# Optimization experiments

Hardware: AMD Instinct MI355X
Metric: run time of the kernel (lower is better)

## Reference

```python
import jax, jax.numpy as jnp
import numpy as np

N_ITERS = 30  # sinkhorn iterations, matching torch default


def sinkhorn(log_alpha, n_iters=N_ITERS):
    # log_alpha: (B, N, K) -> approximately doubly-stochastic (B, N, K)
    x = log_alpha - jnp.max(log_alpha, axis=(-2, -1), keepdims=True)
    x = jnp.exp(x)
    for _ in range(n_iters):
        x = x / (jnp.sum(x, axis=-1, keepdims=True) + 1e-8)  # row normalize
        x = x / (jnp.sum(x, axis=-2, keepdims=True) + 1e-8)  # col normalize
    return x


def greedy_unique_argmax(scores):
    # scores: (B, N, K) with N == K. Returns hard permutation matrix (B, N, K).
    B, N, K = scores.shape

    def one(s):  # s: (N, K)
        order = jnp.argsort(-s.reshape(-1))  # flat indices, descending score

        def body(carry, idx):
            used_r, used_c, assign = carry
            r = idx // K
            c = idx % K
            take = jnp.logical_not(used_r[r] | used_c[c])
            used_r = used_r.at[r].set(used_r[r] | take)
            used_c = used_c.at[c].set(used_c[c] | take)
            assign = assign.at[r].set(jnp.where(take, c, assign[r]))
            return (used_r, used_c, assign), None

        init = (jnp.zeros((N,), jnp.bool_),
                jnp.zeros((K,), jnp.bool_),
                jnp.full((N,), 0, jnp.int32))
        (_, _, assign), _ = jax.lax.scan(body, init, order)
        return jax.nn.one_hot(assign, K, dtype=s.dtype)

    return jax.vmap(one)(scores)


def setup_inputs() -> dict:
    key = jax.random.key(0)
    B, N, K = 4096, 64, 64
    cell_logits = jax.random.normal(key, (B, N, K), dtype=jnp.float32)
    pos_temp = jnp.asarray(1.1, dtype=jnp.float32)  # softplus(pos_temp_raw)+1e-6 at init
    return {"cell_logits": cell_logits, "pos_temp": pos_temp}


def reference(cell_logits, pos_temp):
    logits = cell_logits / (pos_temp + 1e-6)
    w_soft = sinkhorn(logits, N_ITERS)
    w_hard = greedy_unique_argmax(jax.lax.stop_gradient(w_soft))
    # straight-through: forward = hard permutation, backward = soft sinkhorn grads
    w = w_hard + (w_soft - jax.lax.stop_gradient(w_soft))
    return w
```

## Files before the change

kernel.cpp:

```cpp
#include <hip/hip_runtime.h>
#include <cstdint>
#include <cstddef>


typedef float f2 __attribute__((ext_vector_type(2)));

__device__ __forceinline__ f2 fma2(f2 a, f2 b, f2 c) {
#if defined(__has_builtin) && __has_builtin(__builtin_elementwise_fma)
    return __builtin_elementwise_fma(a, b, c);
#else
    f2 r; r.x = __builtin_fmaf(a.x, b.x, c.x); r.y = __builtin_fmaf(a.y, b.y, c.y);
    return r;
#endif
}

__global__ void __launch_bounds__(64)
__attribute__((amdgpu_waves_per_eu(1)))
sinkhorn_perm_kernel(const float* __restrict__ logits,
                     const float* __restrict__ ptemp,
                     float* __restrict__ out)
{
    __shared__ __attribute__((aligned(16))) float bufU[64];
    __shared__ __attribute__((aligned(16))) float bufV[64];

    const int b    = blockIdx.x;
    const int lane = threadIdx.x;
    const float* base = logits + (size_t)b * 4096;

    const float T    = ptemp[0] + 1e-6f;
    const float invT = 1.0f / T;

    f2 row2[32];
    {
        const float4* rp = (const float4*)(base + lane * 64);
        #pragma unroll
        for (int t = 0; t < 16; ++t) {
            float4 q = rp[t];
            row2[2*t+0].x = __fmul_rn(q.x, invT);
            row2[2*t+0].y = __fmul_rn(q.y, invT);
            row2[2*t+1].x = __fmul_rn(q.z, invT);
            row2[2*t+1].y = __fmul_rn(q.w, invT);
        }
    }

    float mx = row2[0].x;
    #pragma unroll
    for (int i = 0; i < 32; ++i) { mx = fmaxf(mx, row2[i].x); mx = fmaxf(mx, row2[i].y); }
    #pragma unroll
    for (int w = 1; w <= 32; w <<= 1)
        mx = fmaxf(mx, __shfl_xor(mx, w, 64));

    #pragma unroll
    for (int i = 0; i < 32; ++i) {
        row2[i].x = __expf(__fsub_rn(row2[i].x, mx));
        row2[i].y = __expf(__fsub_rn(row2[i].y, mx));
    }

    float col[64];
    #pragma unroll
    for (int i = 0; i < 64; ++i) {
        float raw = base[i * 64 + lane];
        col[i] = __expf(__fsub_rn(__fmul_rn(raw, invT), mx));
    }

    const float4* bu4 = (const float4*)bufU;
    const float4* bv4 = (const float4*)bufV;

    float u = 1.0f, v = 1.0f;
    for (int it = 0; it < 30; ++it) {
        bufV[lane] = v;
        f2 A0 = {0.f, 0.f}, A1 = {0.f, 0.f};
        #pragma unroll
        for (int t = 0; t < 16; ++t) {
            float4 q = bv4[t];
            f2 qa = { q.x, q.y };
            f2 qb = { q.z, q.w };
            A0 = fma2(row2[2*t+0], qa, A0);
            A1 = fma2(row2[2*t+1], qb, A1);
        }
        float rs = __fadd_rn(__fadd_rn(A0.x, A0.y), __fadd_rn(A1.x, A1.y));
        u = u / __fadd_rn(__fmul_rn(u, rs), 1e-8f);

        bufU[lane] = u;
        A0 = (f2){0.f, 0.f}; A1 = (f2){0.f, 0.f};
        #pragma unroll
        for (int t = 0; t < 16; ++t) {
            float4 q = bu4[t];
            f2 ca = { col[4*t+0], col[4*t+1] };
            f2 cb = { col[4*t+2], col[4*t+3] };
            f2 qa = { q.x, q.y };
            f2 qb = { q.z, q.w };
            A0 = fma2(ca, qa, A0);
            A1 = fma2(cb, qb, A1);
        }
        float cs = __fadd_rn(__fadd_rn(A0.x, A0.y), __fadd_rn(A1.x, A1.y));
        v = v / __fadd_rn(__fmul_rn(v, cs), 1e-8f);
    }

    #pragma unroll
    for (int t = 0; t < 16; ++t) {
        float4 q = bu4[t];
        col[4*t+0] = __fmul_rn(__fmul_rn(col[4*t+0], q.x), v);
        col[4*t+1] = __fmul_rn(__fmul_rn(col[4*t+1], q.y), v);
        col[4*t+2] = __fmul_rn(__fmul_rn(col[4*t+2], q.z), v);
        col[4*t+3] = __fmul_rn(__fmul_rn(col[4*t+3], q.w), v);
    }
    bufV[lane] = v;
    #pragma unroll
    for (int t = 0; t < 16; ++t) {
        float4 q = bv4[t];
        row2[2*t+0].x = __fmul_rn(__fmul_rn(row2[2*t+0].x, u), q.x);
        row2[2*t+0].y = __fmul_rn(__fmul_rn(row2[2*t+0].y, u), q.y);
        row2[2*t+1].x = __fmul_rn(__fmul_rn(row2[2*t+1].x, u), q.z);
        row2[2*t+1].y = __fmul_rn(__fmul_rn(row2[2*t+1].y, u), q.w);
    }

    unsigned long long rowmask = ~0ull;
    unsigned long long colmask = ~0ull;
    int mycol  = 0;
    int rounds = 0;

    while (rowmask && rounds < 64) {
        ++rounds;

        float rbv = 0.0f; int rbj = 0;
        #pragma unroll
        for (int j = 0; j < 64; ++j) {
            unsigned sm = ((colmask >> j) & 1ull) ? 0xFFFFFFFFu : 0u;
            float sv = (j & 1) ? row2[j >> 1].y : row2[j >> 1].x;
            float s  = __uint_as_float(__float_as_uint(sv) & sm);
            if (s > rbv) { rbv = s; rbj = j; }
        }

        float cbv = 0.0f; int cbi = 0;
        #pragma unroll
        for (int i = 0; i < 64; ++i) {
            unsigned sm = ((rowmask >> i) & 1ull) ? 0xFFFFFFFFu : 0u;
            float s  = __uint_as_float(__float_as_uint(col[i]) & sm);
            if (s > cbv) { cbv = s; cbi = i; }
        }

        int gr = __builtin_amdgcn_ds_bpermute(rbj << 2, cbi);
        int gc = __builtin_amdgcn_ds_bpermute(cbi << 2, rbj);
        bool aR = (rowmask >> lane) & 1ull;
        bool aC = (colmask >> lane) & 1ull;
        bool mr = aR && (gr == lane);
        bool mc = aC && (gc == lane);
        if (mr) mycol = rbj;
        rowmask &= ~__ballot(mr);
        colmask &= ~__ballot(mc);
    }

    float* orow = out + (size_t)b * 4096 + lane * 64;
    #pragma unroll
    for (int t = 0; t < 16; ++t) {
        float4 q;
        q.x = (4*t+0 == mycol) ? 1.0f : 0.0f;
        q.y = (4*t+1 == mycol) ? 1.0f : 0.0f;
        q.z = (4*t+2 == mycol) ? 1.0f : 0.0f;
        q.w = (4*t+3 == mycol) ? 1.0f : 0.0f;
        ((float4*)orow)[t] = q;
    }
}

extern "C" void kernel_launch(void* const* d_in, const int* in_sizes, int n_in,
                              void* d_out, int out_size, void* d_ws, size_t ws_size,
                              hipStream_t stream) {
    const float* logits = (const float*)d_in[0];
    const float* ptemp  = (const float*)d_in[1];
    float* out = (float*)d_out;
    const int B = in_sizes[0] / 4096;
    sinkhorn_perm_kernel<<<B, 64, 0, stream>>>(logits, ptemp, out);
}
```

Before: 179.7 us.

## Process two batch matrices per wavefront to interleave independent Sinkhorn chains

Each 64-lane block now handles two batch entries, keeping both row and column copies in registers and interleaving their Sinkhorn iterations and greedy assignment rounds. The aim is more instruction-level parallelism to hide LDS and dependency latency in the serial iteration chain, with half as many blocks. The cost is roughly doubled register use (about 256+ VGPRs for the data), which risks spilling or lower occupancy, and the assignment loop runs to the maximum round count of the two matrices.

```diff
diff --git a/kernel.cpp b/kernel.cpp
--- a/kernel.cpp
+++ b/kernel.cpp
@@ -18,148 +18,222 @@
 __attribute__((amdgpu_waves_per_eu(1)))
 sinkhorn_perm_kernel(const float* __restrict__ logits,
                      const float* __restrict__ ptemp,
-                     float* __restrict__ out)
+                     float* __restrict__ out,
+                     int B)
 {
-    __shared__ __attribute__((aligned(16))) float bufU[64];
-    __shared__ __attribute__((aligned(16))) float bufV[64];
-
-    const int b    = blockIdx.x;
+    __shared__ __attribute__((aligned(16))) float bufUA[64];
+    __shared__ __attribute__((aligned(16))) float bufVA[64];
+    __shared__ __attribute__((aligned(16))) float bufUB[64];
+    __shared__ __attribute__((aligned(16))) float bufVB[64];
+
     const int lane = threadIdx.x;
-    const float* base = logits + (size_t)b * 4096;
+    const int bA   = blockIdx.x * 2;
+    const int bB   = bA + 1;
+    const bool hasB = (bB < B);
+    const float* baseA = logits + (size_t)bA * 4096;
+    const float* baseB = logits + (size_t)(hasB ? bB : bA) * 4096;
 
     const float T    = ptemp[0] + 1e-6f;
     const float invT = 1.0f / T;
 
-    f2 row2[32];
+    f2 rowA[32], rowB[32];
     {
-        const float4* rp = (const float4*)(base + lane * 64);
-        #pragma unroll
-        for (int t = 0; t < 16; ++t) {
-            float4 q = rp[t];
-            row2[2*t+0].x = __fmul_rn(q.x, invT);
-            row2[2*t+0].y = __fmul_rn(q.y, invT);
-            row2[2*t+1].x = __fmul_rn(q.z, invT);
-            row2[2*t+1].y = __fmul_rn(q.w, invT);
-        }
-    }
-
-    float mx = row2[0].x;
-    #pragma unroll
-    for (int i = 0; i < 32; ++i) { mx = fmaxf(mx, row2[i].x); mx = fmaxf(mx, row2[i].y); }
-    #pragma unroll
-    for (int w = 1; w <= 32; w <<= 1)
-        mx = fmaxf(mx, __shfl_xor(mx, w, 64));
-
+        const float4* rpA = (const float4*)(baseA + lane * 64);
+        const float4* rpB = (const float4*)(baseB + lane * 64);
+        #pragma unroll
+        for (int t = 0; t < 16; ++t) {
+            float4 qa = rpA[t];
+            float4 qb = rpB[t];
+            rowA[2*t+0].x = __fmul_rn(qa.x, invT);
+            rowA[2*t+0].y = __fmul_rn(qa.y, invT);
+            rowA[2*t+1].x = __fmul_rn(qa.z, invT);
+            rowA[2*t+1].y = __fmul_rn(qa.w, invT);
+            rowB[2*t+0].x = __fmul_rn(qb.x, invT);
+            rowB[2*t+0].y = __fmul_rn(qb.y, invT);
+            rowB[2*t+1].x = __fmul_rn(qb.z, invT);
+            rowB[2*t+1].y = __fmul_rn(qb.w, invT);
+        }
+    }
+
+    float mxA = rowA[0].x, mxB = rowB[0].x;
     #pragma unroll
     for (int i = 0; i < 32; ++i) {
-        row2[i].x = __expf(__fsub_rn(row2[i].x, mx));
-        row2[i].y = __expf(__fsub_rn(row2[i].y, mx));
-    }
-
-    float col[64];
+        mxA = fmaxf(mxA, rowA[i].x); mxA = fmaxf(mxA, rowA[i].y);
+        mxB = fmaxf(mxB, rowB[i].x); mxB = fmaxf(mxB, rowB[i].y);
+    }
+    #pragma unroll
+    for (int w = 1; w <= 32; w <<= 1) {
+        mxA = fmaxf(mxA, __shfl_xor(mxA, w, 64));
+        mxB = fmaxf(mxB, __shfl_xor(mxB, w, 64));
+    }
+
+    #pragma unroll
+    for (int i = 0; i < 32; ++i) {
+        rowA[i].x = __expf(__fsub_rn(rowA[i].x, mxA));
+        rowA[i].y = __expf(__fsub_rn(rowA[i].y, mxA));
+        rowB[i].x = __expf(__fsub_rn(rowB[i].x, mxB));
+        rowB[i].y = __expf(__fsub_rn(rowB[i].y, mxB));
+    }
+
+    float colA[64], colB[64];
     #pragma unroll
     for (int i = 0; i < 64; ++i) {
-        float raw = base[i * 64 + lane];
-        col[i] = __expf(__fsub_rn(__fmul_rn(raw, invT), mx));
-    }
-
-    const float4* bu4 = (const float4*)bufU;
-    const float4* bv4 = (const float4*)bufV;
-
-    float u = 1.0f, v = 1.0f;
+        float ra = baseA[i * 64 + lane];
+        float rb = baseB[i * 64 + lane];
+        colA[i] = __expf(__fsub_rn(__fmul_rn(ra, invT), mxA));
+        colB[i] = __expf(__fsub_rn(__fmul_rn(rb, invT), mxB));
+    }
+
+    const float4* buA4 = (const float4*)bufUA;
+    const float4* bvA4 = (const float4*)bufVA;
+    const float4* buB4 = (const float4*)bufUB;
+    const float4* bvB4 = (const float4*)bufVB;
+
+    float uA = 1.0f, vA = 1.0f, uB = 1.0f, vB = 1.0f;
     for (int it = 0; it < 30; ++it) {
-        bufV[lane] = v;
-        f2 A0 = {0.f, 0.f}, A1 = {0.f, 0.f};
-        #pragma unroll
-        for (int t = 0; t < 16; ++t) {
-            float4 q = bv4[t];
-            f2 qa = { q.x, q.y };
-            f2 qb = { q.z, q.w };
-            A0 = fma2(row2[2*t+0], qa, A0);
-            A1 = fma2(row2[2*t+1], qb, A1);
-        }
-        float rs = __fadd_rn(__fadd_rn(A0.x, A0.y), __fadd_rn(A1.x, A1.y));
-        u = u / __fadd_rn(__fmul_rn(u, rs), 1e-8f);
-
-        bufU[lane] = u;
-        A0 = (f2){0.f, 0.f}; A1 = (f2){0.f, 0.f};
-        #pragma unroll
-        for (int t = 0; t < 16; ++t) {
-            float4 q = bu4[t];
-            f2 ca = { col[4*t+0], col[4*t+1] };
-            f2 cb = { col[4*t+2], col[4*t+3] };
-            f2 qa = { q.x, q.y };
-            f2 qb = { q.z, q.w };
-            A0 = fma2(ca, qa, A0);
-            A1 = fma2(cb, qb, A1);
-        }
-        float cs = __fadd_rn(__fadd_rn(A0.x, A0.y), __fadd_rn(A1.x, A1.y));
-        v = v / __fadd_rn(__fmul_rn(v, cs), 1e-8f);
+        bufVA[lane] = vA;
+        bufVB[lane] = vB;
+        f2 Aa0 = {0.f,0.f}, Aa1 = {0.f,0.f}, Ab0 = {0.f,0.f}, Ab1 = {0.f,0.f};
+        #pragma unroll
+        for (int t = 0; t < 16; ++t) {
+            float4 qa = bvA4[t];
+            float4 qb = bvB4[t];
+            f2 qa0 = { qa.x, qa.y }, qa1 = { qa.z, qa.w };
+            f2 qb0 = { qb.x, qb.y }, qb1 = { qb.z, qb.w };
+            Aa0 = fma2(rowA[2*t+0], qa0, Aa0);
+            Aa1 = fma2(rowA[2*t+1], qa1, Aa1);
+            Ab0 = fma2(rowB[2*t+0], qb0, Ab0);
+            Ab1 = fma2(rowB[2*t+1], qb1, Ab1);
+        }
+        float rsA = __fadd_rn(__fadd_rn(Aa0.x, Aa0.y), __fadd_rn(Aa1.x, Aa1.y));
+        float rsB = __fadd_rn(__fadd_rn(Ab0.x, Ab0.y), __fadd_rn(Ab1.x, Ab1.y));
+        uA = uA / __fadd_rn(__fmul_rn(uA, rsA), 1e-8f);
+        uB = uB / __fadd_rn(__fmul_rn(uB, rsB), 1e-8f);
+
+        bufUA[lane] = uA;
+        bufUB[lane] = uB;
+        Aa0 = (f2){0.f,0.f}; Aa1 = (f2){0.f,0.f};
+        Ab0 = (f2){0.f,0.f}; Ab1 = (f2){0.f,0.f};
+        #pragma unroll
+        for (int t = 0; t < 16; ++t) {
+            float4 qa = buA4[t];
+            float4 qb = buB4[t];
+            f2 ca0 = { colA[4*t+0], colA[4*t+1] }, ca1 = { colA[4*t+2], colA[4*t+3] };
+            f2 cb0 = { colB[4*t+0], colB[4*t+1] }, cb1 = { colB[4*t+2], colB[4*t+3] };
+            f2 qa0 = { qa.x, qa.y }, qa1 = { qa.z, qa.w };
+            f2 qb0 = { qb.x, qb.y }, qb1 = { qb.z, qb.w };
+            Aa0 = fma2(ca0, qa0, Aa0);
+            Aa1 = fma2(ca1, qa1, Aa1);
+            Ab0 = fma2(cb0, qb0, Ab0);
+            Ab1 = fma2(cb1, qb1, Ab1);
+        }
+        float csA = __fadd_rn(__fadd_rn(Aa0.x, Aa0.y), __fadd_rn(Aa1.x, Aa1.y));
+        float csB = __fadd_rn(__fadd_rn(Ab0.x, Ab0.y), __fadd_rn(Ab1.x, Ab1.y));
+        vA = vA / __fadd_rn(__fmul_rn(vA, csA), 1e-8f);
+        vB = vB / __fadd_rn(__fmul_rn(vB, csB), 1e-8f);
     }
 
     #pragma unroll
     for (int t = 0; t < 16; ++t) {
-        float4 q = bu4[t];
-        col[4*t+0] = __fmul_rn(__fmul_rn(col[4*t+0], q.x), v);
-        col[4*t+1] = __fmul_rn(__fmul_rn(col[4*t+1], q.y), v);
-        col[4*t+2] = __fmul_rn(__fmul_rn(col[4*t+2], q.z), v);
-        col[4*t+3] = __fmul_rn(__fmul_rn(col[4*t+3], q.w), v);
-    }
-    bufV[lane] = v;
+        float4 qa = buA4[t];
+        float4 qb = buB4[t];
+        colA[4*t+0] = __fmul_rn(__fmul_rn(colA[4*t+0], qa.x), vA);
+        colA[4*t+1] = __fmul_rn(__fmul_rn(colA[4*t+1], qa.y), vA);
+        colA[4*t+2] = __fmul_rn(__fmul_rn(colA[4*t+2], qa.z), vA);
+        colA[4*t+3] = __fmul_rn(__fmul_rn(colA[4*t+3], qa.w), vA);
+        colB[4*t+0] = __fmul_rn(__fmul_rn(colB[4*t+0], qb.x), vB);
+        colB[4*t+1] = __fmul_rn(__fmul_rn(colB[4*t+1], qb.y), vB);
+        colB[4*t+2] = __fmul_rn(__fmul_rn(colB[4*t+2], qb.z), vB);
+        colB[4*t+3] = __fmul_rn(__fmul_rn(colB[4*t+3], qb.w), vB);
+    }
+    bufVA[lane] = vA;
+    bufVB[lane] = vB;
     #pragma unroll
     for (int t = 0; t < 16; ++t) {
-        float4 q = bv4[t];
-        row2[2*t+0].x = __fmul_rn(__fmul_rn(row2[2*t+0].x, u), q.x);
-        row2[2*t+0].y = __fmul_rn(__fmul_rn(row2[2*t+0].y, u), q.y);
-        row2[2*t+1].x = __fmul_rn(__fmul_rn(row2[2*t+1].x, u), q.z);
-        row2[2*t+1].y = __fmul_rn(__fmul_rn(row2[2*t+1].y, u), q.w);
-    }
-
-    unsigned long long rowmask = ~0ull;
-    unsigned long long colmask = ~0ull;
-    int mycol  = 0;
+        float4 qa = bvA4[t];
+        float4 qb = bvB4[t];
+        rowA[2*t+0].x = __fmul_rn(__fmul_rn(rowA[2*t+0].x, uA), qa.x);
+        rowA[2*t+0].y = __fmul_rn(__fmul_rn(rowA[2*t+0].y, uA), qa.y);
+        rowA[2*t+1].x = __fmul_rn(__fmul_rn(rowA[2*t+1].x, uA), qa.z);
+        rowA[2*t+1].y = __fmul_rn(__fmul_rn(rowA[2*t+1].y, uA), qa.w);
+        rowB[2*t+0].x = __fmul_rn(__fmul_rn(rowB[2*t+0].x, uB), qb.x);
+        rowB[2*t+0].y = __fmul_rn(__fmul_rn(rowB[2*t+0].y, uB), qb.y);
+        rowB[2*t+1].x = __fmul_rn(__fmul_rn(rowB[2*t+1].x, uB), qb.z);
+        rowB[2*t+1].y = __fmul_rn(__fmul_rn(rowB[2*t+1].y, uB), qb.w);
+    }
+
+    unsigned long long rmA = ~0ull, cmA = ~0ull;
+    unsigned long long rmB = hasB ? ~0ull : 0ull;
+    unsigned long long cmB = hasB ? ~0ull : 0ull;
+    int mycolA = 0, mycolB = 0;
     int rounds = 0;
 
-    while (rowmask && rounds < 64) {
+    while ((rmA | rmB) && rounds < 64) {
         ++rounds;
 
-        float rbv = 0.0f; int rbj = 0;
+        float rbvA = 0.0f, rbvB = 0.0f; int rbjA = 0, rbjB = 0;
         #pragma unroll
         for (int j = 0; j < 64; ++j) {
-            unsigned sm = ((colmask >> j) & 1ull) ? 0xFFFFFFFFu : 0u;
-            float sv = (j & 1) ? row2[j >> 1].y : row2[j >> 1].x;
-            float s  = __uint_as_float(__float_as_uint(sv) & sm);
-            if (s > rbv) { rbv = s; rbj = j; }
-        }
-
-        float cbv = 0.0f; int cbi = 0;
+            unsigned smA = ((cmA >> j) & 1ull) ? 0xFFFFFFFFu : 0u;
+            unsigned smB = ((cmB >> j) & 1ull) ? 0xFFFFFFFFu : 0u;
+            float svA = (j & 1) ? rowA[j >> 1].y : rowA[j >> 1].x;
+            float svB = (j & 1) ? rowB[j >> 1].y : rowB[j >> 1].x;
+            float sA = __uint_as_float(__float_as_uint(svA) & smA);
+            float sB = __uint_as_float(__float_as_uint(svB) & smB);
+            if (sA > rbvA) { rbvA = sA; rbjA = j; }
+            if (sB > rbvB) { rbvB = sB; rbjB = j; }
+        }
+
+        float cbvA = 0.0f, cbvB = 0.0f; int cbiA = 0, cbiB = 0;
         #pragma unroll
         for (int i = 0; i < 64; ++i) {
-            unsigned sm = ((rowmask >> i) & 1ull) ? 0xFFFFFFFFu : 0u;
-            float s  = __uint_as_float(__float_as_uint(col[i]) & sm);
-            if (s > cbv) { cbv = s; cbi = i; }
-        }
-
-        int gr = __builtin_amdgcn_ds_bpermute(rbj << 2, cbi);
-        int gc = __builtin_amdgcn_ds_bpermute(cbi << 2, rbj);
-        bool aR = (rowmask >> lane) & 1ull;
-        bool aC = (colmask >> lane) & 1ull;
-        bool mr = aR && (gr == lane);
-        bool mc = aC && (gc == lane);
-        if (mr) mycol = rbj;
-        rowmask &= ~__ballot(mr);
-        colmask &= ~__ballot(mc);
-    }
-
-    float* orow = out + (size_t)b * 4096 + lane * 64;
-    #pragma unroll
-    for (int t = 0; t < 16; ++t) {
-        float4 q;
-        q.x = (4*t+0 == mycol) ? 1.0f : 0.0f;
-        q.y = (4*t+1 == mycol) ? 1.0f : 0.0f;
-        q.z = (4*t+2 == mycol) ? 1.0f : 0.0f;
-        q.w = (4*t+3 == mycol) ? 1.0f : 0.0f;
-        ((float4*)orow)[t] = q;
+            unsigned smA = ((rmA >> i) & 1ull) ? 0xFFFFFFFFu : 0u;
+            unsigned smB = ((rmB >> i) & 1ull) ? 0xFFFFFFFFu : 0u;
+            float sA = __uint_as_float(__float_as_uint(colA[i]) & smA);
+            float sB = __uint_as_float(__float_as_uint(colB[i]) & smB);
+            if (sA > cbvA) { cbvA = sA; cbiA = i; }
+            if (sB > cbvB) { cbvB = sB; cbiB = i; }
+        }
+
+        int grA = __builtin_amdgcn_ds_bpermute(rbjA << 2, cbiA);
+        int gcA = __builtin_amdgcn_ds_bpermute(cbiA << 2, rbjA);
+        int grB = __builtin_amdgcn_ds_bpermute(rbjB << 2, cbiB);
+        int gcB = __builtin_amdgcn_ds_bpermute(cbiB << 2, rbjB);
+        bool aRA = (rmA >> lane) & 1ull, aCA = (cmA >> lane) & 1ull;
+        bool aRB = (rmB >> lane) & 1ull, aCB = (cmB >> lane) & 1ull;
+        bool mrA = aRA && (grA == lane);
+        bool mcA = aCA && (gcA == lane);
+        bool mrB = aRB && (grB == lane);
+        bool mcB = aCB && (gcB == lane);
+        if (mrA) mycolA = rbjA;
+        if (mrB) mycolB = rbjB;
+        rmA &= ~__ballot(mrA); cmA &= ~__ballot(mcA);
+        rmB &= ~__ballot(mrB); cmB &= ~__ballot(mcB);
+    }
+
+    {
+        float* orow = out + (size_t)bA * 4096 + lane * 64;
+        #pragma unroll
+        for (int t = 0; t < 16; ++t) {
+            float4 q;
+            q.x = (4*t+0 == mycolA) ? 1.0f : 0.0f;
+            q.y = (4*t+1 == mycolA) ? 1.0f : 0.0f;
+            q.z = (4*t+2 == mycolA) ? 1.0f : 0.0f;
+            q.w = (4*t+3 == mycolA) ? 1.0f : 0.0f;
+            ((float4*)orow)[t] = q;
+        }
+    }
+    if (hasB) {
+        float* orow = out + (size_t)bB * 4096 + lane * 64;
+        #pragma unroll
+        for (int t = 0; t < 16; ++t) {
+            float4 q;
+            q.x = (4*t+0 == mycolB) ? 1.0f : 0.0f;
+            q.y = (4*t+1 == mycolB) ? 1.0f : 0.0f;
+            q.z = (4*t+2 == mycolB) ? 1.0f : 0.0f;
+            q.w = (4*t+3 == mycolB) ? 1.0f : 0.0f;
+            ((float4*)orow)[t] = q;
+        }
     }
 }
 
@@ -170,5 +244,6 @@
     const float* ptemp  = (const float*)d_in[1];
     float* out = (float*)d_out;
     const int B = in_sizes[0] / 4096;
-    sinkhorn_perm_kernel<<<B, 64, 0, stream>>>(logits, ptemp, out);
+    const int G = (B + 1) / 2;
+    sinkhorn_perm_kernel<<<G, 64, 0, stream>>>(logits, ptemp, out, B);
 }
```

Measured after the change: 383.2 us. 2.13x slower.

## Build column copy via swizzled LDS transpose and split argmax scans into four chains

Applied to the files above, without the earlier changes.

Instead of re-reading the logits from global memory column-wise and recomputing exp, each lane writes its exponentiated row into a 16KB swizzled LDS tile, and the column values are read back from it. This removes 64 strided global loads and 64 exps per lane, at the cost of 16KB of LDS per block. The per-round row and column argmax loops in the greedy matching are also split into four independent compare chains merged at the end. This shortens the serial dependency chain, with a small cost in extra registers.

```diff
diff --git a/kernel.cpp b/kernel.cpp
--- a/kernel.cpp
+++ b/kernel.cpp
@@ -20,6 +20,7 @@
                      const float* __restrict__ ptemp,
                      float* __restrict__ out)
 {
+    __shared__ __attribute__((aligned(16))) float ldsT[4096];
     __shared__ __attribute__((aligned(16))) float bufU[64];
     __shared__ __attribute__((aligned(16))) float bufV[64];
 
@@ -56,11 +57,25 @@
         row2[i].y = __expf(__fsub_rn(row2[i].y, mx));
     }
 
+    {
+        const unsigned swz4  = (unsigned)((lane & 7) << 4);
+        const unsigned vbase = ((unsigned)lane << 8) + swz4;
+        #pragma unroll
+        for (int t = 0; t < 16; ++t) {
+            float4 q;
+            q.x = row2[2*t+0].x; q.y = row2[2*t+0].y;
+            q.z = row2[2*t+1].x; q.w = row2[2*t+1].y;
+            *(float4*)((char*)ldsT + (vbase ^ (unsigned)(t << 4))) = q;
+        }
+    }
     float col[64];
-    #pragma unroll
-    for (int i = 0; i < 64; ++i) {
-        float raw = base[i * 64 + lane];
-        col[i] = __expf(__fsub_rn(__fmul_rn(raw, invT), mx));
+    {
+        int a8[8];
+        #pragma unroll
+        for (int g = 0; g < 8; ++g) a8[g] = ((lane ^ (g << 2)) << 2);
+        #pragma unroll
+        for (int i = 0; i < 64; ++i)
+            col[i] = *(const float*)((const char*)ldsT + a8[i & 7] + (i << 8));
     }
 
     const float4* bu4 = (const float4*)bufU;
@@ -123,22 +138,77 @@
     while (rowmask && rounds < 64) {
         ++rounds;
 
-        float rbv = 0.0f; int rbj = 0;
-        #pragma unroll
-        for (int j = 0; j < 64; ++j) {
-            unsigned sm = ((colmask >> j) & 1ull) ? 0xFFFFFFFFu : 0u;
-            float sv = (j & 1) ? row2[j >> 1].y : row2[j >> 1].x;
-            float s  = __uint_as_float(__float_as_uint(sv) & sm);
-            if (s > rbv) { rbv = s; rbj = j; }
-        }
-
-        float cbv = 0.0f; int cbi = 0;
-        #pragma unroll
-        for (int i = 0; i < 64; ++i) {
-            unsigned sm = ((rowmask >> i) & 1ull) ? 0xFFFFFFFFu : 0u;
-            float s  = __uint_as_float(__float_as_uint(col[i]) & sm);
-            if (s > cbv) { cbv = s; cbi = i; }
-        }
+        float rv0 = 0.f, rv1 = 0.f, rv2 = 0.f, rv3 = 0.f;
+        int   rj0 = 0,   rj1 = 16,  rj2 = 32,  rj3 = 48;
+        #pragma unroll
+        for (int k = 0; k < 16; ++k) {
+            {
+                const int j = k;
+                unsigned sm = ((colmask >> j) & 1ull) ? 0xFFFFFFFFu : 0u;
+                float sv = (j & 1) ? row2[j >> 1].y : row2[j >> 1].x;
+                float s  = __uint_as_float(__float_as_uint(sv) & sm);
+                if (s > rv0) { rv0 = s; rj0 = j; }
+            }
+            {
+                const int j = 16 + k;
+                unsigned sm = ((colmask >> j) & 1ull) ? 0xFFFFFFFFu : 0u;
+                float sv = (j & 1) ? row2[j >> 1].y : row2[j >> 1].x;
+                float s  = __uint_as_float(__float_as_uint(sv) & sm);
+                if (s > rv1) { rv1 = s; rj1 = j; }
+            }
+            {
+                const int j = 32 + k;
+                unsigned sm = ((colmask >> j) & 1ull) ? 0xFFFFFFFFu : 0u;
+                float sv = (j & 1) ? row2[j >> 1].y : row2[j >> 1].x;
+                float s  = __uint_as_float(__float_as_uint(sv) & sm);
+                if (s > rv2) { rv2 = s; rj2 = j; }
+            }
+            {
+                const int j = 48 + k;
+                unsigned sm = ((colmask >> j) & 1ull) ? 0xFFFFFFFFu : 0u;
+                float sv = (j & 1) ? row2[j >> 1].y : row2[j >> 1].x;
+                float s  = __uint_as_float(__float_as_uint(sv) & sm);
+                if (s > rv3) { rv3 = s; rj3 = j; }
+            }
+        }
+        if (rv1 > rv0) { rv0 = rv1; rj0 = rj1; }
+        if (rv2 > rv0) { rv0 = rv2; rj0 = rj2; }
+        if (rv3 > rv0) { rv0 = rv3; rj0 = rj3; }
+        const int rbj = rj0;
+
+        float cv0 = 0.f, cv1 = 0.f, cv2 = 0.f, cv3 = 0.f;
+        int   ci0 = 0,   ci1 = 16,  ci2 = 32,  ci3 = 48;
+        #pragma unroll
+        for (int k = 0; k < 16; ++k) {
+            {
+                const int i = k;
+                unsigned sm = ((rowmask >> i) & 1ull) ? 0xFFFFFFFFu : 0u;
+                float s  = __uint_as_float(__float_as_uint(col[i]) & sm);
+                if (s > cv0) { cv0 = s; ci0 = i; }
+            }
+            {
+                const int i = 16 + k;
+                unsigned sm = ((rowmask >> i) & 1ull) ? 0xFFFFFFFFu : 0u;
+                float s  = __uint_as_float(__float_as_uint(col[i]) & sm);
+                if (s > cv1) { cv1 = s; ci1 = i; }
+            }
+            {
+                const int i = 32 + k;
+                unsigned sm = ((rowmask >> i) & 1ull) ? 0xFFFFFFFFu : 0u;
+                float s  = __uint_as_float(__float_as_uint(col[i]) & sm);
+                if (s > cv2) { cv2 = s; ci2 = i; }
+            }
+            {
+                const int i = 48 + k;
+                unsigned sm = ((rowmask >> i) & 1ull) ? 0xFFFFFFFFu : 0u;
+                float s  = __uint_as_float(__float_as_uint(col[i]) & sm);
+                if (s > cv3) { cv3 = s; ci3 = i; }
+            }
+        }
+        if (cv1 > cv0) { cv0 = cv1; ci0 = ci1; }
+        if (cv2 > cv0) { cv0 = cv2; ci0 = ci2; }
+        if (cv3 > cv0) { cv0 = cv3; ci0 = ci3; }
+        const int cbi = ci0;
 
         int gr = __builtin_amdgcn_ds_bpermute(rbj << 2, cbi);
         int gc = __builtin_amdgcn_ds_bpermute(cbi << 2, rbj);
```

New measurement: 280.7 us. 1.56x slower.
